# Kernel tuning notes

Measured on AMD Instinct MI355X. Metric: run time of the kernel, lower is better.

Reference implementation:

```python
import jax, jax.numpy as jnp
import numpy as np


def setup_inputs() -> dict:
    key = jax.random.key(0)
    k1, k2, k3, k4 = jax.random.split(key, 4)
    B, T, K = 256, 2048, 48
    logits = jax.random.normal(k1, (B, T, K), dtype=jnp.float32)
    transition_params = jax.random.normal(k2, (K, K), dtype=jnp.float32)
    targets = jax.random.randint(k3, (B, T), 0, K, dtype=jnp.int32)
    input_lengths = jax.random.randint(k4, (B,), 0, T, dtype=jnp.int32)
    return {"logits": logits, "transition_params": transition_params,
            "targets": targets, "input_lengths": input_lengths}


def _crf_log_likelihood(logits, transition_params, targets, input_lengths):
    B, T, K = logits.shape
    mask = (jnp.arange(T)[None, :] < input_lengths[:, None]).astype(logits.dtype)  # [B,T]

    # unary score: gather logits at target tags, masked sum over time
    unary = jnp.take_along_axis(logits, targets[..., None].astype(jnp.int32), axis=2)[..., 0]  # [B,T]
    unary_score = jnp.sum(unary * mask, axis=1)

    # binary score: transitions between consecutive tags, masked by mask[:,1:]
    binary = transition_params[targets[:, :-1], targets[:, 1:]]  # [B,T-1]
    binary_score = jnp.sum(binary * mask[:, 1:], axis=1)

    # log norm via forward algorithm (sequential logsumexp scan)
    alpha0 = logits[:, 0, :]  # [B,K]

    def step(alpha, logit_t):
        # alpha: [B,K] prev tag scores; logit_t: [B,K]
        scores = alpha[:, :, None] + transition_params[None, :, :]  # [B,K,K]
        new_alpha = logit_t + jax.nn.logsumexp(scores, axis=1)      # [B,K]
        return new_alpha, new_alpha

    _, alphas_rest = jax.lax.scan(step, alpha0, jnp.swapaxes(logits[:, 1:, :], 0, 1))
    all_alphas = jnp.concatenate([alpha0[None], alphas_rest], axis=0)  # [T,B,K]
    all_alphas = jnp.swapaxes(all_alphas, 0, 1)                        # [B,T,K]

    last_index = jnp.maximum(0, input_lengths - 1).astype(jnp.int32)   # [B]
    final_alpha = jnp.take_along_axis(all_alphas, last_index[:, None, None], axis=1)[:, 0, :]  # [B,K]
    log_norm = jax.nn.logsumexp(final_alpha, axis=1)
    log_norm = jnp.where(input_lengths <= 0, jnp.zeros_like(log_norm), log_norm)

    return unary_score + binary_score - log_norm  # [B]


def reference(logits, transition_params, targets, input_lengths):
    return _crf_log_likelihood(logits, transition_params, targets, input_lengths)
```

## Files before the change

kernel.cpp:

```cpp
#include <hip/hip_runtime.h>
#include <hip/hip_bf16.h>
#include <math.h>

#define TT   2048
#define KK   48
#define SEG  128
#define NFULL 15
#define KP   68

typedef __attribute__((ext_vector_type(8))) short bf16x8;
typedef __attribute__((ext_vector_type(4))) float f32x4;
typedef __attribute__((ext_vector_type(4))) unsigned int u32x4;
typedef unsigned short ushort_t;

union FragU { u32x4 u; bf16x8 h; };

__device__ __forceinline__ float rlf(float x, int l) {
    return __uint_as_float((unsigned)__builtin_amdgcn_readlane((int)__float_as_uint(x), l));
}
__device__ __forceinline__ unsigned pk2(float a, float b) {
    __hip_bfloat162 h = __float22bfloat162_rn(make_float2(a, b));
    return *(unsigned*)&h;
}
__device__ __forceinline__ unsigned pk2a(float a, float b) {
    unsigned r;
    asm("v_cvt_pk_bf16_f32 %0, %1, %2" : "=v"(r) : "v"(a), "v"(b));
    return r;
}

__global__ __launch_bounds__(64) void crf_seg_kernel(
    const float* __restrict__ logits,
    const float* __restrict__ trans,
    const int*   __restrict__ lens,
    ushort_t*    __restrict__ Qout,
    float*       __restrict__ sigout)
{
    const int b    = blockIdx.x;
    const int seg  = blockIdx.y;
    const int job  = b * 16 + seg;
    const int lane = threadIdx.x;
    const int c = lane & 15, g = lane >> 4;

    int t0, t1;
    if (seg < NFULL) { t0 = SEG * seg + 1; t1 = SEG * seg + SEG; }
    else {
        int L  = lens[b];
        int nf = (L >= 2) ? (L - 1) / SEG : 0;
        if (nf > NFULL) nf = NFULL;
        t0 = SEG * nf + 1; t1 = L - 1;
    }

    __shared__ float    eLs[2][64];
    __shared__ ushort_t Qst[KK * KP];

    FragU A[3][2];
    #pragma unroll
    for (int mt = 0; mt < 3; ++mt) {
        const int r = 16 * mt + c;
        #pragma unroll
        for (int q = 0; q < 2; ++q) {
            #pragma unroll
            for (int ep = 0; ep < 4; ++ep) {
                float v0, v1;
                { int e = 2 * ep;     int kk = 32 * q + 16 * (e >> 2) + 4 * g + (e & 3);
                  v0 = (kk < KK) ? __expf(trans[kk * KK + r]) : 0.f; }
                { int e = 2 * ep + 1; int kk = 32 * q + 16 * (e >> 2) + 4 * g + (e & 3);
                  v1 = (kk < KK) ? __expf(trans[kk * KK + r]) : 0.f; }
                A[mt][q].u[ep] = pk2(v0, v1);
            }
        }
    }

    FragU Bf[3][2];
    #pragma unroll
    for (int nt = 0; nt < 3; ++nt) {
        const int n = 16 * nt + c;
        #pragma unroll
        for (int q = 0; q < 2; ++q) {
            #pragma unroll
            for (int ep = 0; ep < 4; ++ep) {
                int e0 = 2 * ep, e1 = 2 * ep + 1;
                int k0 = 32 * q + 16 * (e0 >> 2) + 4 * g + (e0 & 3);
                int k1 = 32 * q + 16 * (e1 >> 2) + 4 * g + (e1 & 3);
                unsigned lo = (k0 == n) ? 0x3F80u : 0u;
                unsigned hi = (k1 == n) ? 0x3F80u : 0u;
                Bf[nt][q].u[ep] = (hi << 16) | lo;
            }
        }
    }

    const float* lg_b = logits + (size_t)b * TT * KK;
    const int jj = (lane < KK) ? lane : 0;
    float sg = 0.f;

    float lg_nxt = lg_b[(t0 + 1) * KK + jj];
    if (lane < KK) eLs[0][lane] = __expf(lg_b[t0 * KK + jj]);
    int par = 0;

    #pragma unroll 1
    for (int t = t0; t <= t1; ++t) {
        f32x4 eL4[3];
        #pragma unroll
        for (int mt = 0; mt < 3; ++mt)
            eL4[mt] = *(const f32x4*)&eLs[par][16 * mt + 4 * g];

        int nrow = t + 2; if (nrow > TT - 1) nrow = TT - 1;
        float lg_pf = lg_b[nrow * KK + jj];
        if (lane < KK) eLs[par ^ 1][lane] = __expf(lg_nxt);

        f32x4 acc[3][3];
        #pragma unroll
        for (int mt = 0; mt < 3; ++mt)
            #pragma unroll
            for (int nt = 0; nt < 3; ++nt) {
                f32x4 z = {0.f, 0.f, 0.f, 0.f};
                f32x4 a1 = __builtin_amdgcn_mfma_f32_16x16x32_bf16(A[mt][0].h, Bf[nt][0].h, z,  0, 0, 0);
                acc[mt][nt] = __builtin_amdgcn_mfma_f32_16x16x32_bf16(A[mt][1].h, Bf[nt][1].h, a1, 0, 0, 0);
            }

        float r  = __uint_as_float((unsigned)__builtin_amdgcn_readfirstlane((int)__float_as_uint(acc[0][0][0])));
        float rr = __builtin_amdgcn_rcpf(r);
        sg += __logf(r);

        f32x4 es0 = eL4[0] * rr, es1 = eL4[1] * rr, es2 = eL4[2] * rr;
        #pragma unroll
        for (int nt = 0; nt < 3; ++nt) {
            f32x4 v0 = acc[0][nt] * es0;
            f32x4 v1 = acc[1][nt] * es1;
            f32x4 v2 = acc[2][nt] * es2;
            Bf[nt][0].u[0] = pk2a(v0[0], v0[1]);
            Bf[nt][0].u[1] = pk2a(v0[2], v0[3]);
            Bf[nt][0].u[2] = pk2a(v1[0], v1[1]);
            Bf[nt][0].u[3] = pk2a(v1[2], v1[3]);
            Bf[nt][1].u[0] = pk2a(v2[0], v2[1]);
            Bf[nt][1].u[1] = pk2a(v2[2], v2[3]);
            Bf[nt][1].u[2] = 0u;
            Bf[nt][1].u[3] = 0u;
        }

        lg_nxt = lg_pf;
        par ^= 1;
    }

    #pragma unroll
    for (int nt = 0; nt < 3; ++nt) {
        ushort_t* basep = &Qst[(16 * nt + c) * KP];
        *(unsigned*)&basep[4 * g]          = Bf[nt][0].u[0];
        *(unsigned*)&basep[4 * g + 2]      = Bf[nt][0].u[1];
        *(unsigned*)&basep[16 + 4 * g]     = Bf[nt][0].u[2];
        *(unsigned*)&basep[16 + 4 * g + 2] = Bf[nt][0].u[3];
        *(unsigned*)&basep[32 + 4 * g]     = Bf[nt][1].u[0];
        *(unsigned*)&basep[32 + 4 * g + 2] = Bf[nt][1].u[1];
    }
    __syncthreads();

    if (lane < KK) {
        const int m = lane;
        unsigned w[24];
        #pragma unroll
        for (int np = 0; np < 24; ++np) {
            unsigned lo = Qst[(2 * np)     * KP + m];
            unsigned hi = Qst[(2 * np + 1) * KP + m];
            w[np] = (hi << 16) | lo;
        }
        ushort_t* dst = Qout + (size_t)job * (KK * KK) + m * KK;
        #pragma unroll
        for (int i4 = 0; i4 < 6; ++i4) {
            uint4 o; o.x = w[4*i4]; o.y = w[4*i4+1]; o.z = w[4*i4+2]; o.w = w[4*i4+3];
            *(uint4*)&dst[8 * i4] = o;
        }
    }
    if (lane == 0) sigout[job] = sg;
}

__global__ __launch_bounds__(64) void crf_comb_kernel(
    const float* __restrict__ logits, const float* __restrict__ trans,
    const int* __restrict__ targets, const int* __restrict__ lens,
    const ushort_t* __restrict__ Qall, const float* __restrict__ sig,
    float* __restrict__ out)
{
    const int b = blockIdx.x, lane = threadIdx.x;
    const int jj = (lane < KK) ? lane : 0;
    const int L = lens[b];

    __shared__ float s_trans[KK * KK];
    for (int k = lane; k < KK * KK; k += 64) s_trans[k] = trans[k];
    __syncthreads();

    const float* lg_b = logits  + (size_t)b * TT * KK;
    const int*   tg_b = targets + (size_t)b * TT;

    float ub = 0.f;
    #pragma unroll 4
    for (int t = lane; t < TT; t += 64) {
        if (t < L) {
            int tg = tg_b[t];
            ub += lg_b[t * KK + tg];
            if (t >= 1) { int tp = tg_b[t - 1]; ub += s_trans[tp * KK + tg]; }
        }
    }
    #pragma unroll
    for (int d = 32; d >= 1; d >>= 1) ub += __shfl_xor(ub, d, 64);

    float log_norm = 0.f;
    if (L > 0) {
        float a0 = lg_b[jj];
        float M  = rlf(a0, 0);
        float s  = (lane < KK) ? __expf(a0 - M) : 0.f;
        int nf = (L >= 2) ? (L - 1) / SEG : 0;
        if (nf > NFULL) nf = NFULL;

        for (int ci = 0; ci <= nf; ++ci) {
            const int job = b * 16 + ((ci < nf) ? ci : NFULL);
            const ushort_t* Qr = Qall + (size_t)job * (KK * KK) + jj * KK;
            unsigned rw[24];
            #pragma unroll
            for (int i4 = 0; i4 < 6; ++i4) {
                uint4 v = *(const uint4*)&Qr[8 * i4];
                rw[4*i4] = v.x; rw[4*i4+1] = v.y; rw[4*i4+2] = v.z; rw[4*i4+3] = v.w;
            }
            float acc = 0.f;
            #pragma unroll
            for (int ip = 0; ip < 24; ++ip) {
                unsigned u = rw[ip];
                float q0 = __uint_as_float(u << 16);
                float q1 = __uint_as_float(u & 0xFFFF0000u);
                acc = fmaf(rlf(s, 2 * ip),     q0, acc);
                acc = fmaf(rlf(s, 2 * ip + 1), q1, acc);
            }
            float r  = rlf(acc, 0);
            float rr = __builtin_amdgcn_rcpf(r);
            s = (lane < KK) ? acc * rr : 0.f;
            M += __logf(r) + sig[job];
        }

        float ssum = (lane < KK) ? s : 0.f;
        #pragma unroll
        for (int d = 32; d >= 1; d >>= 1) ssum += __shfl_xor(ssum, d, 64);
        log_norm = M + __logf(ssum);
    }

    if (lane == 0) out[b] = (L <= 0) ? 0.f : (ub - log_norm);
}

__global__ __launch_bounds__(64) void crf_fwd_fallback(
    const float* __restrict__ logits, const float* __restrict__ trans,
    const int* __restrict__ targets, const int* __restrict__ lens,
    float* __restrict__ out)
{
    const int b = blockIdx.x, lane = threadIdx.x;
    const int jj = (lane < KK) ? lane : 0;
    const int L = lens[b];
    __shared__ float s_trans[KK * KK];
    for (int k = lane; k < KK * KK; k += 64) s_trans[k] = trans[k];
    float et[KK];
    #pragma unroll
    for (int i = 0; i < KK; ++i) et[i] = __expf(trans[i * KK + jj]);
    __syncthreads();
    const float* lg_b = logits + (size_t)b * TT * KK;
    const int* tg_b = targets + (size_t)b * TT;
    float ub = 0.f;
    for (int t = lane; t < TT; t += 64) {
        if (t < L) {
            int tg = tg_b[t];
            ub += lg_b[t * KK + tg];
            if (t >= 1) { int tp = tg_b[t - 1]; ub += s_trans[tp * KK + tg]; }
        }
    }
    #pragma unroll
    for (int d = 32; d >= 1; d >>= 1) ub += __shfl_xor(ub, d, 64);
    float a0 = lg_b[jj];
    float M = rlf(a0, 0);
    float s = (lane < KK) ? __expf(a0 - M) : 0.f;
    float sC = s, MC = M;
    const int Lm1 = L - 1;
    float pf[8];
    #pragma unroll
    for (int u = 0; u < 8; ++u) pf[u] = lg_b[(1 + u) * KK + jj];
    #pragma unroll 1
    for (int cc = 0; cc < 256; ++cc) {
        #pragma unroll
        for (int u = 0; u < 8; ++u) {
            const int t = 1 + cc * 8 + u;
            float lg = pf[u];
            int nrow = t + 8; if (nrow > TT - 1) nrow = TT - 1;
            pf[u] = lg_b[nrow * KK + jj];
            float eL = __expf(lg);
            float ac0 = 0.f, ac1 = 0.f, ac2 = 0.f, ac3 = 0.f;
            #pragma unroll
            for (int i = 0; i < KK; i += 4) {
                float s0 = rlf(s, i), s1 = rlf(s, i+1), s2 = rlf(s, i+2), s3 = rlf(s, i+3);
                ac0 = fmaf(s0, et[i], ac0);   ac1 = fmaf(s1, et[i+1], ac1);
                ac2 = fmaf(s2, et[i+2], ac2); ac3 = fmaf(s3, et[i+3], ac3);
            }
            float e = ((ac0 + ac1) + (ac2 + ac3)) * eL;
            bool cap = (t == Lm1);
            sC = cap ? e : sC;  MC = cap ? M : MC;
            float r = rlf(e, 0);
            s = e * __builtin_amdgcn_rcpf(r);
            M += __logf(r);
        }
    }
    float ssum = (lane < KK) ? sC : 0.f;
    #pragma unroll
    for (int d = 32; d >= 1; d >>= 1) ssum += __shfl_xor(ssum, d, 64);
    float log_norm = MC + __logf(ssum);
    if (lane == 0) out[b] = (L <= 0) ? 0.f : (ub - log_norm);
}

extern "C" void kernel_launch(void* const* d_in, const int* in_sizes, int n_in,
                              void* d_out, int out_size, void* d_ws, size_t ws_size,
                              hipStream_t stream) {
    const float* logits  = (const float*)d_in[0];
    const float* trans   = (const float*)d_in[1];
    const int*   targets = (const int*)  d_in[2];
    const int*   lens    = (const int*)  d_in[3];
    float*       out     = (float*)d_out;
    const int B = in_sizes[3];

    const size_t qbytes = (size_t)B * 16 * KK * KK * sizeof(ushort_t);
    const size_t need   = qbytes + (size_t)B * 16 * sizeof(float);
    if (ws_size >= need) {
        ushort_t* Qout = (ushort_t*)d_ws;
        float*    sig  = (float*)((char*)d_ws + qbytes);
        crf_seg_kernel<<<dim3(B, 16), 64, 0, stream>>>(logits, trans, lens, Qout, sig);
        crf_comb_kernel<<<B, 64, 0, stream>>>(logits, trans, targets, lens, Qout, sig, out);
    } else {
        crf_fwd_fallback<<<B, 64, 0, stream>>>(logits, trans, targets, lens, out);
    }
}
```

Baseline: 202.5 us.

## Unroll recurrence 8x with deeper logits prefetch and packed fp32 multiplies

The sequential segment loop is unrolled by 8 through a STEP macro, with an 8-entry register ring that prefetches logits 8 steps ahead instead of 1. The scaling multiplies now use v_pk_mul_f32 through inline asm. A guarded tail chunk masks out steps past the segment end. The aim is to hide global-load latency and cut loop and VALU overhead on the latency-bound serial chain, at the cost of more registers and code size.

```diff
diff --git a/kernel.cpp b/kernel.cpp
--- a/kernel.cpp
+++ b/kernel.cpp
@@ -10,10 +10,12 @@
 
 typedef __attribute__((ext_vector_type(8))) short bf16x8;
 typedef __attribute__((ext_vector_type(4))) float f32x4;
+typedef __attribute__((ext_vector_type(2))) float f32x2;
 typedef __attribute__((ext_vector_type(4))) unsigned int u32x4;
 typedef unsigned short ushort_t;
 
 union FragU { u32x4 u; bf16x8 h; };
+union Q4   { f32x4 v; f32x2 h[2]; };
 
 __device__ __forceinline__ float rlf(float x, int l) {
     return __uint_as_float((unsigned)__builtin_amdgcn_readlane((int)__float_as_uint(x), l));
@@ -26,6 +28,11 @@
     unsigned r;
     asm("v_cvt_pk_bf16_f32 %0, %1, %2" : "=v"(r) : "v"(a), "v"(b));
     return r;
+}
+__device__ __forceinline__ f32x2 pkmul(f32x2 a, f32x2 b) {
+    f32x2 d;
+    asm("v_pk_mul_f32 %0, %1, %2" : "=v"(d) : "v"(a), "v"(b));
+    return d;
 }
 
 __global__ __launch_bounds__(64) void crf_seg_kernel(
@@ -92,55 +99,101 @@
     const float* lg_b = logits + (size_t)b * TT * KK;
     const int jj = (lane < KK) ? lane : 0;
     float sg = 0.f;
-
-    float lg_nxt = lg_b[(t0 + 1) * KK + jj];
-    if (lane < KK) eLs[0][lane] = __expf(lg_b[t0 * KK + jj]);
+    const int nsteps = t1 - t0 + 1;
+
+#define STEP(u_, G_)                                                          \
+    {                                                                         \
+        const int i = 8 * cs + (u_);                                          \
+        f32x4 eL4[3];                                                         \
+        _Pragma("unroll")                                                     \
+        for (int mt = 0; mt < 3; ++mt)                                        \
+            eL4[mt] = *(const f32x4*)&eLs[par][16 * mt + 4 * g];              \
+        float lgn = pf[((u_) + 1) & 7];                                       \
+        int nr = t0 + i + 9; if (nr > TT - 1) nr = TT - 1;                    \
+        pf[((u_) + 1) & 7] = lg_b[nr * KK + jj];                              \
+        if (lane < KK) eLs[par ^ 1][lane] = __expf(lgn);                      \
+        f32x4 acc[3][3];                                                      \
+        _Pragma("unroll")                                                     \
+        for (int mt = 0; mt < 3; ++mt)                                        \
+            _Pragma("unroll")                                                 \
+            for (int nt = 0; nt < 3; ++nt) {                                  \
+                f32x4 z = {0.f, 0.f, 0.f, 0.f};                               \
+                f32x4 a1 = __builtin_amdgcn_mfma_f32_16x16x32_bf16(           \
+                               A[mt][0].h, Bf[nt][0].h, z, 0, 0, 0);          \
+                acc[mt][nt] = __builtin_amdgcn_mfma_f32_16x16x32_bf16(        \
+                               A[mt][1].h, Bf[nt][1].h, a1, 0, 0, 0);         \
+            }                                                                 \
+        float r = __uint_as_float((unsigned)__builtin_amdgcn_readfirstlane(   \
+                      (int)__float_as_uint(acc[0][0][0])));                   \
+        float rr = __builtin_amdgcn_rcpf(r);                                  \
+        float logr = __logf(r);                                               \
+        bool jk = G_ ? (i >= nsteps) : false;                                 \
+        sg += jk ? 0.f : logr;                                                \
+        f32x2 rr2 = {rr, rr};                                                 \
+        Q4 es0, es1, es2;                                                     \
+        { Q4 e0_; e0_.v = eL4[0]; es0.h[0] = pkmul(e0_.h[0], rr2);            \
+                                  es0.h[1] = pkmul(e0_.h[1], rr2); }          \
+        { Q4 e1_; e1_.v = eL4[1]; es1.h[0] = pkmul(e1_.h[0], rr2);            \
+                                  es1.h[1] = pkmul(e1_.h[1], rr2); }          \
+        { Q4 e2_; e2_.v = eL4[2]; es2.h[0] = pkmul(e2_.h[0], rr2);            \
+                                  es2.h[1] = pkmul(e2_.h[1], rr2); }          \
+        _Pragma("unroll")                                                     \
+        for (int nt = 0; nt < 3; ++nt) {                                      \
+            Q4 a0_, a1_, a2_;                                                 \
+            a0_.v = acc[0][nt]; a1_.v = acc[1][nt]; a2_.v = acc[2][nt];       \
+            f32x2 v00 = pkmul(a0_.h[0], es0.h[0]);                            \
+            f32x2 v01 = pkmul(a0_.h[1], es0.h[1]);                            \
+            f32x2 v10 = pkmul(a1_.h[0], es1.h[0]);                            \
+            f32x2 v11 = pkmul(a1_.h[1], es1.h[1]);                            \
+            f32x2 v20 = pkmul(a2_.h[0], es2.h[0]);                            \
+            f32x2 v21 = pkmul(a2_.h[1], es2.h[1]);                            \
+            unsigned w0 = pk2a(v00[0], v00[1]);                               \
+            unsigned w1 = pk2a(v01[0], v01[1]);                               \
+            unsigned w2 = pk2a(v10[0], v10[1]);                               \
+            unsigned w3 = pk2a(v11[0], v11[1]);                               \
+            unsigned w4 = pk2a(v20[0], v20[1]);                               \
+            unsigned w5 = pk2a(v21[0], v21[1]);                               \
+            if (G_) {                                                         \
+                Bf[nt][0].u[0] = jk ? Bf[nt][0].u[0] : w0;                    \
+                Bf[nt][0].u[1] = jk ? Bf[nt][0].u[1] : w1;                    \
+                Bf[nt][0].u[2] = jk ? Bf[nt][0].u[2] : w2;                    \
+                Bf[nt][0].u[3] = jk ? Bf[nt][0].u[3] : w3;                    \
+                Bf[nt][1].u[0] = jk ? Bf[nt][1].u[0] : w4;                    \
+                Bf[nt][1].u[1] = jk ? Bf[nt][1].u[1] : w5;                    \
+            } else {                                                          \
+                Bf[nt][0].u[0] = w0; Bf[nt][0].u[1] = w1;                     \
+                Bf[nt][0].u[2] = w2; Bf[nt][0].u[3] = w3;                     \
+                Bf[nt][1].u[0] = w4; Bf[nt][1].u[1] = w5;                     \
+            }                                                                 \
+            Bf[nt][1].u[2] = 0u; Bf[nt][1].u[3] = 0u;                         \
+        }                                                                     \
+        par ^= 1;                                                             \
+    }
+
     int par = 0;
-
-    #pragma unroll 1
-    for (int t = t0; t <= t1; ++t) {
-        f32x4 eL4[3];
-        #pragma unroll
-        for (int mt = 0; mt < 3; ++mt)
-            eL4[mt] = *(const f32x4*)&eLs[par][16 * mt + 4 * g];
-
-        int nrow = t + 2; if (nrow > TT - 1) nrow = TT - 1;
-        float lg_pf = lg_b[nrow * KK + jj];
-        if (lane < KK) eLs[par ^ 1][lane] = __expf(lg_nxt);
-
-        f32x4 acc[3][3];
-        #pragma unroll
-        for (int mt = 0; mt < 3; ++mt)
-            #pragma unroll
-            for (int nt = 0; nt < 3; ++nt) {
-                f32x4 z = {0.f, 0.f, 0.f, 0.f};
-                f32x4 a1 = __builtin_amdgcn_mfma_f32_16x16x32_bf16(A[mt][0].h, Bf[nt][0].h, z,  0, 0, 0);
-                acc[mt][nt] = __builtin_amdgcn_mfma_f32_16x16x32_bf16(A[mt][1].h, Bf[nt][1].h, a1, 0, 0, 0);
-            }
-
-        float r  = __uint_as_float((unsigned)__builtin_amdgcn_readfirstlane((int)__float_as_uint(acc[0][0][0])));
-        float rr = __builtin_amdgcn_rcpf(r);
-        sg += __logf(r);
-
-        f32x4 es0 = eL4[0] * rr, es1 = eL4[1] * rr, es2 = eL4[2] * rr;
-        #pragma unroll
-        for (int nt = 0; nt < 3; ++nt) {
-            f32x4 v0 = acc[0][nt] * es0;
-            f32x4 v1 = acc[1][nt] * es1;
-            f32x4 v2 = acc[2][nt] * es2;
-            Bf[nt][0].u[0] = pk2a(v0[0], v0[1]);
-            Bf[nt][0].u[1] = pk2a(v0[2], v0[3]);
-            Bf[nt][0].u[2] = pk2a(v1[0], v1[1]);
-            Bf[nt][0].u[3] = pk2a(v1[2], v1[3]);
-            Bf[nt][1].u[0] = pk2a(v2[0], v2[1]);
-            Bf[nt][1].u[1] = pk2a(v2[2], v2[3]);
-            Bf[nt][1].u[2] = 0u;
-            Bf[nt][1].u[3] = 0u;
-        }
-
-        lg_nxt = lg_pf;
-        par ^= 1;
-    }
+    if (nsteps > 0) {
+        if (lane < KK) eLs[0][lane] = __expf(lg_b[t0 * KK + jj]);
+        float pf[8];
+        #pragma unroll
+        for (int j = 1; j < 8; ++j) {
+            int rj = t0 + j; if (rj > TT - 1) rj = TT - 1;
+            pf[j] = lg_b[rj * KK + jj];
+        }
+        { int rj = t0 + 8; if (rj > TT - 1) rj = TT - 1; pf[0] = lg_b[rj * KK + jj]; }
+
+        const int nchunks = (nsteps + 7) / 8;
+        #pragma unroll 1
+        for (int cs = 0; cs < nchunks - 1; ++cs) {
+            STEP(0, false) STEP(1, false) STEP(2, false) STEP(3, false)
+            STEP(4, false) STEP(5, false) STEP(6, false) STEP(7, false)
+        }
+        {
+            const int cs = nchunks - 1;
+            STEP(0, true) STEP(1, true) STEP(2, true) STEP(3, true)
+            STEP(4, true) STEP(5, true) STEP(6, true) STEP(7, true)
+        }
+    }
+#undef STEP
 
     #pragma unroll
     for (int nt = 0; nt < 3; ++nt) {
```

After: 199.7 us. About the same (-1.4%).

## Interleave two independent segment chains per wavefront with shorter segments

Applied to the files above, without the earlier changes.

Each wavefront now advances two independent forward-algorithm segments in lockstep, with segment length reduced from 128 to 64 and 32 segments per sequence, so MFMA latency of one chain can be hidden behind the other. Renormalisation happens every 4 steps instead of every step, logits are prefetched 4 steps ahead, and the loop is unrolled by 8. The final partial segment B masks inactive steps via selects. In exchange the combine kernel has twice as many 48x48 matrices to fold in, register pressure roughly doubles, and skipping per-step rescaling risks bf16 range drift over four steps.

```diff
diff --git a/kernel.cpp b/kernel.cpp
--- a/kernel.cpp
+++ b/kernel.cpp
@@ -4,8 +4,6 @@
 
 #define TT   2048
 #define KK   48
-#define SEG  128
-#define NFULL 15
 #define KP   68
 
 typedef __attribute__((ext_vector_type(8))) short bf16x8;
@@ -28,29 +26,34 @@
     return r;
 }
 
-__global__ __launch_bounds__(64) void crf_seg_kernel(
+template <int SEGT, int NSEGT>
+__global__ __launch_bounds__(64, 4) void crf_seg2_kernel(
     const float* __restrict__ logits,
     const float* __restrict__ trans,
     const int*   __restrict__ lens,
     ushort_t*    __restrict__ Qout,
     float*       __restrict__ sigout)
 {
+    constexpr int NFULLT = NSEGT - 1;
     const int b    = blockIdx.x;
-    const int seg  = blockIdx.y;
-    const int job  = b * 16 + seg;
+    const int segA = 2 * blockIdx.y;
+    const int segB = segA + 1;
+    const int jobA = b * NSEGT + segA;
+    const int jobB = b * NSEGT + segB;
     const int lane = threadIdx.x;
     const int c = lane & 15, g = lane >> 4;
 
-    int t0, t1;
-    if (seg < NFULL) { t0 = SEG * seg + 1; t1 = SEG * seg + SEG; }
+    const int t0A = SEGT * segA + 1;
+    int t0B, nstepsB;
+    if (segB < NFULLT) { t0B = SEGT * segB + 1; nstepsB = SEGT; }
     else {
         int L  = lens[b];
-        int nf = (L >= 2) ? (L - 1) / SEG : 0;
-        if (nf > NFULL) nf = NFULL;
-        t0 = SEG * nf + 1; t1 = L - 1;
-    }
-
-    __shared__ float    eLs[2][64];
+        int nf = (L >= 2) ? (L - 1) / SEGT : 0;
+        if (nf > NFULLT) nf = NFULLT;
+        t0B = SEGT * nf + 1; nstepsB = L - t0B;
+    }
+
+    __shared__ float    eLs[2][128];
     __shared__ ushort_t Qst[KK * KP];
 
     FragU A[3][2];
@@ -71,7 +74,7 @@
         }
     }
 
-    FragU Bf[3][2];
+    FragU BfA[3][2], BfB[3][2];
     #pragma unroll
     for (int nt = 0; nt < 3; ++nt) {
         const int n = 16 * nt + c;
@@ -84,101 +87,168 @@
                 int k1 = 32 * q + 16 * (e1 >> 2) + 4 * g + (e1 & 3);
                 unsigned lo = (k0 == n) ? 0x3F80u : 0u;
                 unsigned hi = (k1 == n) ? 0x3F80u : 0u;
-                Bf[nt][q].u[ep] = (hi << 16) | lo;
+                BfA[nt][q].u[ep] = (hi << 16) | lo;
+                BfB[nt][q].u[ep] = (hi << 16) | lo;
             }
         }
     }
 
     const float* lg_b = logits + (size_t)b * TT * KK;
     const int jj = (lane < KK) ? lane : 0;
-    float sg = 0.f;
-
-    float lg_nxt = lg_b[(t0 + 1) * KK + jj];
-    if (lane < KK) eLs[0][lane] = __expf(lg_b[t0 * KK + jj]);
+    float sgA = 0.f, sgB = 0.f;
+
+    f32x4 z4 = {0.f, 0.f, 0.f, 0.f};
+    asm("" : "+v"(z4));
+
+#define MFMA6(Y0_, Y1_, Y2_, BFA_, NT_)                                       \
+    Y0_ = __builtin_amdgcn_mfma_f32_16x16x32_bf16(A[0][0].h, BFA_[NT_][0].h, z4, 0, 0, 0); \
+    Y0_ = __builtin_amdgcn_mfma_f32_16x16x32_bf16(A[0][1].h, BFA_[NT_][1].h, Y0_, 0, 0, 0); \
+    Y1_ = __builtin_amdgcn_mfma_f32_16x16x32_bf16(A[1][0].h, BFA_[NT_][0].h, z4, 0, 0, 0); \
+    Y1_ = __builtin_amdgcn_mfma_f32_16x16x32_bf16(A[1][1].h, BFA_[NT_][1].h, Y1_, 0, 0, 0); \
+    Y2_ = __builtin_amdgcn_mfma_f32_16x16x32_bf16(A[2][0].h, BFA_[NT_][0].h, z4, 0, 0, 0); \
+    Y2_ = __builtin_amdgcn_mfma_f32_16x16x32_bf16(A[2][1].h, BFA_[NT_][1].h, Y2_, 0, 0, 0);
+
+#define SCL(Y0_, Y1_, Y2_, BFA_, NT_, EOFF_, RR_, RN_, GB_, JK_)              \
+    {                                                                         \
+        f32x4 e0 = *(const f32x4*)&eLs[par][(EOFF_) + 4 * g];                 \
+        f32x4 e1 = *(const f32x4*)&eLs[par][(EOFF_) + 16 + 4 * g];            \
+        f32x4 e2 = *(const f32x4*)&eLs[par][(EOFF_) + 32 + 4 * g];            \
+        if (RN_) { e0 *= (RR_); e1 *= (RR_); e2 *= (RR_); }                   \
+        f32x4 w0 = Y0_ * e0, w1 = Y1_ * e1, w2 = Y2_ * e2;                    \
+        unsigned n0 = pk2a(w0[0], w0[1]);                                     \
+        unsigned n1 = pk2a(w0[2], w0[3]);                                     \
+        unsigned n2 = pk2a(w1[0], w1[1]);                                     \
+        unsigned n3 = pk2a(w1[2], w1[3]);                                     \
+        unsigned n4 = pk2a(w2[0], w2[1]);                                     \
+        unsigned n5 = pk2a(w2[2], w2[3]);                                     \
+        if (GB_) {                                                            \
+            BFA_[NT_][0].u[0] = (JK_) ? BFA_[NT_][0].u[0] : n0;               \
+            BFA_[NT_][0].u[1] = (JK_) ? BFA_[NT_][0].u[1] : n1;               \
+            BFA_[NT_][0].u[2] = (JK_) ? BFA_[NT_][0].u[2] : n2;               \
+            BFA_[NT_][0].u[3] = (JK_) ? BFA_[NT_][0].u[3] : n3;               \
+            BFA_[NT_][1].u[0] = (JK_) ? BFA_[NT_][1].u[0] : n4;               \
+            BFA_[NT_][1].u[1] = (JK_) ? BFA_[NT_][1].u[1] : n5;               \
+        } else {                                                              \
+            BFA_[NT_][0].u[0] = n0; BFA_[NT_][0].u[1] = n1;                   \
+            BFA_[NT_][0].u[2] = n2; BFA_[NT_][0].u[3] = n3;                   \
+            BFA_[NT_][1].u[0] = n4; BFA_[NT_][1].u[1] = n5;                   \
+        }                                                                     \
+    }
+
+#define STEPP(u_, RN_)                                                        \
+    {                                                                         \
+        const int i = 8 * cs + (u_);                                          \
+        float lgnA = pfA[((u_) + 1) & 3];                                     \
+        int nrA = t0A + i + 5; if (nrA > TT - 1) nrA = TT - 1;                \
+        pfA[((u_) + 1) & 3] = lg_b[nrA * KK + jj];                            \
+        float lgnB = pfB[((u_) + 1) & 3];                                     \
+        int nrB = t0B + i + 5; if (nrB > TT - 1) nrB = TT - 1;                \
+        pfB[((u_) + 1) & 3] = lg_b[nrB * KK + jj];                            \
+        if (lane < KK) {                                                      \
+            eLs[par ^ 1][lane]      = __expf(lgnA);                           \
+            eLs[par ^ 1][64 + lane] = __expf(lgnB);                           \
+        }                                                                     \
+        const bool jkB = (i >= nstepsB);                                      \
+        f32x4 yA0, yA1, yA2, yB0, yB1, yB2;                                   \
+        float rrA = 1.f, rrB = 1.f;                                           \
+        MFMA6(yA0, yA1, yA2, BfA, 0)                                          \
+        MFMA6(yB0, yB1, yB2, BfB, 0)                                          \
+        if (RN_) {                                                            \
+            float rA_ = rlf(yA0[0], 0);                                       \
+            rrA = __builtin_amdgcn_rcpf(rA_);                                 \
+            sgA += __logf(rA_);                                               \
+            float rB_ = rlf(yB0[0], 0);                                       \
+            rrB = __builtin_amdgcn_rcpf(rB_);                                 \
+            sgB += jkB ? 0.f : __logf(rB_);                                   \
+        }                                                                     \
+        SCL(yA0, yA1, yA2, BfA, 0, 0,  rrA, RN_, false, false)                \
+        SCL(yB0, yB1, yB2, BfB, 0, 64, rrB, RN_, true,  jkB)                  \
+        MFMA6(yA0, yA1, yA2, BfA, 1)                                          \
+        MFMA6(yB0, yB1, yB2, BfB, 1)                                          \
+        SCL(yA0, yA1, yA2, BfA, 1, 0,  rrA, RN_, false, false)                \
+        SCL(yB0, yB1, yB2, BfB, 1, 64, rrB, RN_, true,  jkB)                  \
+        MFMA6(yA0, yA1, yA2, BfA, 2)                                          \
+        MFMA6(yB0, yB1, yB2, BfB, 2)                                          \
+        SCL(yA0, yA1, yA2, BfA, 2, 0,  rrA, RN_, false, false)                \
+        SCL(yB0, yB1, yB2, BfB, 2, 64, rrB, RN_, true,  jkB)                  \
+        par ^= 1;                                                             \
+    }
+
     int par = 0;
-
-    #pragma unroll 1
-    for (int t = t0; t <= t1; ++t) {
-        f32x4 eL4[3];
+    {
+        if (lane < KK) {
+            eLs[0][lane]      = __expf(lg_b[t0A * KK + jj]);
+            int r0B = t0B; if (r0B > TT - 1) r0B = TT - 1;
+            eLs[0][64 + lane] = __expf(lg_b[r0B * KK + jj]);
+        }
+        float pfA[4], pfB[4];
         #pragma unroll
-        for (int mt = 0; mt < 3; ++mt)
-            eL4[mt] = *(const f32x4*)&eLs[par][16 * mt + 4 * g];
-
-        int nrow = t + 2; if (nrow > TT - 1) nrow = TT - 1;
-        float lg_pf = lg_b[nrow * KK + jj];
-        if (lane < KK) eLs[par ^ 1][lane] = __expf(lg_nxt);
-
-        f32x4 acc[3][3];
-        #pragma unroll
-        for (int mt = 0; mt < 3; ++mt)
-            #pragma unroll
-            for (int nt = 0; nt < 3; ++nt) {
-                f32x4 z = {0.f, 0.f, 0.f, 0.f};
-                f32x4 a1 = __builtin_amdgcn_mfma_f32_16x16x32_bf16(A[mt][0].h, Bf[nt][0].h, z,  0, 0, 0);
-                acc[mt][nt] = __builtin_amdgcn_mfma_f32_16x16x32_bf16(A[mt][1].h, Bf[nt][1].h, a1, 0, 0, 0);
-            }
-
-        float r  = __uint_as_float((unsigned)__builtin_amdgcn_readfirstlane((int)__float_as_uint(acc[0][0][0])));
-        float rr = __builtin_amdgcn_rcpf(r);
-        sg += __logf(r);
-
-        f32x4 es0 = eL4[0] * rr, es1 = eL4[1] * rr, es2 = eL4[2] * rr;
-        #pragma unroll
-        for (int nt = 0; nt < 3; ++nt) {
-            f32x4 v0 = acc[0][nt] * es0;
-            f32x4 v1 = acc[1][nt] * es1;
-            f32x4 v2 = acc[2][nt] * es2;
-            Bf[nt][0].u[0] = pk2a(v0[0], v0[1]);
-            Bf[nt][0].u[1] = pk2a(v0[2], v0[3]);
-            Bf[nt][0].u[2] = pk2a(v1[0], v1[1]);
-            Bf[nt][0].u[3] = pk2a(v1[2], v1[3]);
-            Bf[nt][1].u[0] = pk2a(v2[0], v2[1]);
-            Bf[nt][1].u[1] = pk2a(v2[2], v2[3]);
-            Bf[nt][1].u[2] = 0u;
-            Bf[nt][1].u[3] = 0u;
-        }
-
-        lg_nxt = lg_pf;
-        par ^= 1;
-    }
-
-    #pragma unroll
-    for (int nt = 0; nt < 3; ++nt) {
-        ushort_t* basep = &Qst[(16 * nt + c) * KP];
-        *(unsigned*)&basep[4 * g]          = Bf[nt][0].u[0];
-        *(unsigned*)&basep[4 * g + 2]      = Bf[nt][0].u[1];
-        *(unsigned*)&basep[16 + 4 * g]     = Bf[nt][0].u[2];
-        *(unsigned*)&basep[16 + 4 * g + 2] = Bf[nt][0].u[3];
-        *(unsigned*)&basep[32 + 4 * g]     = Bf[nt][1].u[0];
-        *(unsigned*)&basep[32 + 4 * g + 2] = Bf[nt][1].u[1];
-    }
-    __syncthreads();
-
-    if (lane < KK) {
-        const int m = lane;
-        unsigned w[24];
-        #pragma unroll
-        for (int np = 0; np < 24; ++np) {
-            unsigned lo = Qst[(2 * np)     * KP + m];
-            unsigned hi = Qst[(2 * np + 1) * KP + m];
-            w[np] = (hi << 16) | lo;
-        }
-        ushort_t* dst = Qout + (size_t)job * (KK * KK) + m * KK;
-        #pragma unroll
-        for (int i4 = 0; i4 < 6; ++i4) {
-            uint4 o; o.x = w[4*i4]; o.y = w[4*i4+1]; o.z = w[4*i4+2]; o.w = w[4*i4+3];
-            *(uint4*)&dst[8 * i4] = o;
-        }
-    }
-    if (lane == 0) sigout[job] = sg;
-}
-
+        for (int j = 1; j < 4; ++j) {
+            int rjA = t0A + j; if (rjA > TT - 1) rjA = TT - 1;
+            pfA[j] = lg_b[rjA * KK + jj];
+            int rjB = t0B + j; if (rjB > TT - 1) rjB = TT - 1;
+            pfB[j] = lg_b[rjB * KK + jj];
+        }
+        { int r4A = t0A + 4; if (r4A > TT - 1) r4A = TT - 1; pfA[0] = lg_b[r4A * KK + jj]; }
+        { int r4B = t0B + 4; if (r4B > TT - 1) r4B = TT - 1; pfB[0] = lg_b[r4B * KK + jj]; }
+
+        constexpr int NCH = SEGT / 8;
+        #pragma unroll 1
+        for (int cs = 0; cs < NCH; ++cs) {
+            STEPP(0, false) STEPP(1, false) STEPP(2, false) STEPP(3, true)
+            STEPP(4, false) STEPP(5, false) STEPP(6, false) STEPP(7, true)
+        }
+    }
+#undef STEPP
+#undef SCL
+#undef MFMA6
+
+#define EPI(BFA_, JOB_, SG_)                                                  \
+    {                                                                         \
+        __syncthreads();                                                      \
+        _Pragma("unroll")                                                     \
+        for (int nt = 0; nt < 3; ++nt) {                                      \
+            ushort_t* basep = &Qst[(16 * nt + c) * KP];                       \
+            *(unsigned*)&basep[4 * g]          = BFA_[nt][0].u[0];            \
+            *(unsigned*)&basep[4 * g + 2]      = BFA_[nt][0].u[1];            \
+            *(unsigned*)&basep[16 + 4 * g]     = BFA_[nt][0].u[2];            \
+            *(unsigned*)&basep[16 + 4 * g + 2] = BFA_[nt][0].u[3];            \
+            *(unsigned*)&basep[32 + 4 * g]     = BFA_[nt][1].u[0];            \
+            *(unsigned*)&basep[32 + 4 * g + 2] = BFA_[nt][1].u[1];            \
+        }                                                                     \
+        __syncthreads();                                                      \
+        if (lane < KK) {                                                      \
+            const int m = lane;                                               \
+            unsigned w[24];                                                   \
+            _Pragma("unroll")                                                 \
+            for (int np = 0; np < 24; ++np) {                                 \
+                unsigned lo = Qst[(2 * np)     * KP + m];                     \
+                unsigned hi = Qst[(2 * np + 1) * KP + m];                     \
+                w[np] = (hi << 16) | lo;                                      \
+            }                                                                 \
+            ushort_t* dst = Qout + (size_t)(JOB_) * (KK * KK) + m * KK;       \
+            _Pragma("unroll")                                                 \
+            for (int i4 = 0; i4 < 6; ++i4) {                                  \
+                uint4 o; o.x = w[4*i4]; o.y = w[4*i4+1];                      \
+                o.z = w[4*i4+2]; o.w = w[4*i4+3];                             \
+                *(uint4*)&dst[8 * i4] = o;                                    \
+            }                                                                 \
+        }                                                                     \
+        if (lane == 0) sigout[JOB_] = SG_;                                    \
+    }
+    EPI(BfA, jobA, sgA)
+    EPI(BfB, jobB, sgB)
+#undef EPI
+}
+
+template <int SEGT, int NSEGT>
 __global__ __launch_bounds__(64) void crf_comb_kernel(
     const float* __restrict__ logits, const float* __restrict__ trans,
     const int* __restrict__ targets, const int* __restrict__ lens,
     const ushort_t* __restrict__ Qall, const float* __restrict__ sig,
     float* __restrict__ out)
 {
+    constexpr int NFULLT = NSEGT - 1;
     const int b = blockIdx.x, lane = threadIdx.x;
     const int jj = (lane < KK) ? lane : 0;
     const int L = lens[b];
@@ -207,11 +277,11 @@
         float a0 = lg_b[jj];
         float M  = rlf(a0, 0);
         float s  = (lane < KK) ? __expf(a0 - M) : 0.f;
-        int nf = (L >= 2) ? (L - 1) / SEG : 0;
-        if (nf > NFULL) nf = NFULL;
+        int nf = (L >= 2) ? (L - 1) / SEGT : 0;
+        if (nf > NFULLT) nf = NFULLT;
 
         for (int ci = 0; ci <= nf; ++ci) {
-            const int job = b * 16 + ((ci < nf) ? ci : NFULL);
+            const int job = b * NSEGT + ((ci < nf) ? ci : NFULLT);
             const ushort_t* Qr = Qall + (size_t)job * (KK * KK) + jj * KK;
             unsigned rw[24];
             #pragma unroll
@@ -318,13 +388,14 @@
     float*       out     = (float*)d_out;
     const int B = in_sizes[3];
 
-    const size_t qbytes = (size_t)B * 16 * KK * KK * sizeof(ushort_t);
-    const size_t need   = qbytes + (size_t)B * 16 * sizeof(float);
-    if (ws_size >= need) {
+    const size_t q64 = (size_t)B * 32 * KK * KK * sizeof(ushort_t);
+    const size_t n64 = q64 + (size_t)B * 32 * sizeof(float);
+
+    if (ws_size >= n64) {
         ushort_t* Qout = (ushort_t*)d_ws;
-        float*    sig  = (float*)((char*)d_ws + qbytes);
-        crf_seg_kernel<<<dim3(B, 16), 64, 0, stream>>>(logits, trans, lens, Qout, sig);
-        crf_comb_kernel<<<B, 64, 0, stream>>>(logits, trans, targets, lens, Qout, sig, out);
+        float*    sig  = (float*)((char*)d_ws + q64);
+        crf_seg2_kernel<64, 32><<<dim3(B, 16), 64, 0, stream>>>(logits, trans, lens, Qout, sig);
+        crf_comb_kernel<64, 32><<<B, 64, 0, stream>>>(logits, trans, targets, lens, Qout, sig, out);
     } else {
         crf_fwd_fallback<<<B, 64, 0, stream>>>(logits, trans, targets, lens, out);
     }
```

New measurement: 575.7 us. 2.84x slower.
